# Kernel tuning notes

Hardware: AMD Instinct MI355X
Metric: run time of the kernel (lower is better)

## Reference

```python
import jax, jax.numpy as jnp
import numpy as np

B = 1024        # batch
S = 2048        # nsampled + 1 (index 0 is the positive label)
E = 128         # emb_size
V = 100000      # vocab = len(tags_weight)


def setup_inputs() -> dict:
    key = jax.random.key(0)
    k1, k2, k3, k4 = jax.random.split(key, 4)
    inputs = jax.random.normal(k1, (B, E), dtype=jnp.float32)
    weight = jax.random.normal(k2, (V, E), dtype=jnp.float32)
    bias = jax.random.normal(k3, (V,), dtype=jnp.float32)
    sample_ids = jax.random.randint(k4, (B, S), 0, V)  # column 0 = positive label
    return {"inputs": inputs, "weight": weight, "bias": bias, "sample_ids": sample_ids}


def reference(inputs, weight, bias, sample_ids):
    # Gather sampled rows: [B, S, E] and [B, S]
    sample_weights = weight[sample_ids]
    sample_bias = bias[sample_ids]
    # Batched dot: logits[b, s] = <inputs[b], sample_weights[b, s]> + bias
    logits = jnp.einsum('be,bse->bs', inputs, sample_weights) + sample_bias
    # CrossEntropyLoss with targets all-zero (positive class is at index 0), mean reduction
    loss = jnp.mean(jax.nn.logsumexp(logits, axis=-1) - logits[:, 0])
    return loss
```

## Files before the change

kernel.cpp:

```cpp
#include <hip/hip_runtime.h>
#include <float.h>
#include <math.h>

#define BATCH 1024
#define NS    2048
#define EMB   128
#define VOCAB 100000
#define THREADS 256

#define PARTS 8
#define PSIZE (VOCAB / PARTS)

#define FCHUNKS 8
#define FSCHUNK (NS / FCHUNKS)
#define ITERSF (FSCHUNK / 64)

#define KSHIFT 40.0f
#define INVB   (1.0f / (float)BATCH)


typedef float floatx2 __attribute__((ext_vector_type(2)));

#if __has_builtin(__builtin_amdgcn_cvt_pk_f32_fp8) && __has_builtin(__builtin_amdgcn_cvt_pk_fp8_f32)
#define USE_FP8_BUILTINS 1
#else
#define USE_FP8_BUILTINS 0
#include <hip/hip_fp8.h>
#endif

__device__ inline floatx2 cvt2_lo(unsigned int w) {
#if USE_FP8_BUILTINS
    return __builtin_amdgcn_cvt_pk_f32_fp8((int)w, false);
#else
    __hip_fp8_e4m3 a, b;
    a.__x = (unsigned char)(w & 0xff);
    b.__x = (unsigned char)((w >> 8) & 0xff);
    floatx2 r; r.x = (float)a; r.y = (float)b; return r;
#endif
}
__device__ inline floatx2 cvt2_hi(unsigned int w) {
#if USE_FP8_BUILTINS
    return __builtin_amdgcn_cvt_pk_f32_fp8((int)w, true);
#else
    __hip_fp8_e4m3 a, b;
    a.__x = (unsigned char)((w >> 16) & 0xff);
    b.__x = (unsigned char)((w >> 24) & 0xff);
    floatx2 r; r.x = (float)a; r.y = (float)b; return r;
#endif
}
__device__ inline unsigned int pack4_fp8(float4 v) {
#if USE_FP8_BUILTINS
    int w = 0;
    w = __builtin_amdgcn_cvt_pk_fp8_f32(v.x, v.y, w, false);
    w = __builtin_amdgcn_cvt_pk_fp8_f32(v.z, v.w, w, true);
    return (unsigned int)w;
#else
    __hip_fp8_e4m3 h0(v.x), h1(v.y), h2(v.z), h3(v.w);
    return (unsigned int)h0.__x | ((unsigned int)h1.__x << 8)
         | ((unsigned int)h2.__x << 16) | ((unsigned int)h3.__x << 24);
#endif
}

__global__ __launch_bounds__(THREADS) void convert_weights_fp8(
    const float* __restrict__ w, unsigned int* __restrict__ w8)
{
    const size_t i = (size_t)blockIdx.x * THREADS + threadIdx.x;
    const float4* src = (const float4*)w;
    float4 a = src[4 * i + 0];
    float4 b = src[4 * i + 1];
    float4 c = src[4 * i + 2];
    float4 d = src[4 * i + 3];
    uint4 o;
    o.x = pack4_fp8(a);
    o.y = pack4_fp8(b);
    o.z = pack4_fp8(c);
    o.w = pack4_fp8(d);
    ((uint4*)w8)[i] = o;
}

__global__ __launch_bounds__(THREADS, 2) void sampled_ce_partial_p(
    const float*        __restrict__ inputs,
    const unsigned int* __restrict__ w8,
    const float*        __restrict__ bias,
    const int*          __restrict__ sample_ids,
    float* __restrict__ pm,
    float* __restrict__ plogit0)
{
    const int blk = blockIdx.x;
    const int p   = blk & (PARTS - 1);
    const int b   = blk >> 3;
    const int t   = threadIdx.x;
    const int lane = t & 63;
    const int e_part = t & 7;
    const int s_sub  = t >> 3;
    const int lo  = p * PSIZE;

    __shared__ float s_in[EMB];
    __shared__ int   s_ids[NS];
    __shared__ int   s_sel[NS];
    __shared__ float s_red[4];
    __shared__ int   s_cnt;
    __shared__ int   s_pos0;

    if (t < EMB / 4) {
        ((float4*)s_in)[t] = ((const float4*)(inputs + (size_t)b * EMB))[t];
    }
    const int4* ids4 = (const int4*)(sample_ids + (size_t)b * NS);
    ((int4*)s_ids)[t]       = ids4[t];
    ((int4*)s_ids)[t + 256] = ids4[t + 256];
    if (t == 0) { s_cnt = 0; s_pos0 = -1; }
    __syncthreads();

#pragma unroll
    for (int c = 0; c < NS / THREADS; ++c) {
        const int pos = c * THREADS + t;
        const int id  = s_ids[pos];
        const bool pred = ((unsigned)(id - lo)) < (unsigned)PSIZE;
        const unsigned long long mask = __ballot(pred);
        int base;
        if (lane == 0) base = atomicAdd(&s_cnt, (int)__popcll(mask));
        base = __shfl(base, 0, 64);
        if (pred) {
            const int slot = base +
                (int)__popcll(mask & ((1ull << lane) - 1ull));
            s_sel[slot] = id;
            if (pos == 0) s_pos0 = slot;
        }
    }
    __syncthreads();

    const int count = s_cnt;
    const int pos0  = s_pos0;

    floatx2 cin[8];
#pragma unroll
    for (int q = 0; q < 8; ++q) {
        const int base = e_part * 16 + 2 * q;
        cin[q].x = s_in[base];
        cin[q].y = s_in[base + 1];
    }

    float lsum = 0.0f;
    for (int base = 0; base < count; base += 8 * 32) {
        int ids8[8];
#pragma unroll
        for (int it = 0; it < 8; ++it) {
            const int slot = base + it * 32 + s_sub;
            ids8[it] = (slot < count) ? s_sel[slot] : lo;
        }
        uint4 q[8];
#pragma unroll
        for (int it = 0; it < 8; ++it)
            q[it] = ((const uint4*)w8)[(size_t)ids8[it] * 8 + e_part];
        float bv[8];
#pragma unroll
        for (int it = 0; it < 8; ++it) bv[it] = bias[ids8[it]];

#pragma unroll
        for (int it = 0; it < 8; ++it) {
            floatx2 a2 = {0.0f, 0.0f};
            a2 += cvt2_lo(q[it].x) * cin[0];
            a2 += cvt2_hi(q[it].x) * cin[1];
            a2 += cvt2_lo(q[it].y) * cin[2];
            a2 += cvt2_hi(q[it].y) * cin[3];
            a2 += cvt2_lo(q[it].z) * cin[4];
            a2 += cvt2_hi(q[it].z) * cin[5];
            a2 += cvt2_lo(q[it].w) * cin[6];
            a2 += cvt2_hi(q[it].w) * cin[7];
            float a = a2.x + a2.y;
            a += __shfl_xor(a, 1, 64);
            a += __shfl_xor(a, 2, 64);
            a += __shfl_xor(a, 4, 64);
            const float logit = a + bv[it];
            const int slot = base + it * 32 + s_sub;
            if (slot < count) {
                lsum += __expf(logit - KSHIFT);
                if (slot == pos0 && e_part == 0) plogit0[b] = logit;
            }
        }
    }

#pragma unroll
    for (int off = 1; off < 64; off <<= 1) lsum += __shfl_xor(lsum, off, 64);
    const int wave = t >> 6;
    if ((t & 63) == 0) s_red[wave] = lsum;
    __syncthreads();
    if (t == 0) {
        pm[blk] = (s_red[0] + s_red[1] + s_red[2] + s_red[3]) * 0.125f;
    }
}

__global__ __launch_bounds__(1024) void sampled_ce_finalize_8(
    const float* __restrict__ pm,
    const float* __restrict__ plogit0,
    float* __restrict__ out)
{
    const int t = threadIdx.x;

    const float4* p4 = (const float4*)(pm + (size_t)t * PARTS);
    const float4 p0 = p4[0];
    const float4 p1 = p4[1];
    const float S = (p0.x + p0.y + p0.z + p0.w) + (p1.x + p1.y + p1.z + p1.w);
    float v = (KSHIFT + __logf(S) - plogit0[t]) * INVB;

#pragma unroll
    for (int off = 1; off < 64; off <<= 1) v += __shfl_xor(v, off, 64);

    __shared__ float s[16];
    if ((t & 63) == 0) s[t >> 6] = v;
    __syncthreads();

    if (t == 0) {
        float sum = 0.0f;
#pragma unroll
        for (int w = 0; w < 16; ++w) sum += s[w];
        out[0] = sum;
    }
}

__global__ __launch_bounds__(THREADS) void sampled_ce_partial_f(
    const float* __restrict__ inputs,
    const float* __restrict__ weight,
    const float* __restrict__ bias,
    const int*   __restrict__ sample_ids,
    float* __restrict__ pm,
    float* __restrict__ pl,
    float* __restrict__ plogit0)
{
    const int blk   = blockIdx.x;
    const int b     = blk >> 3;
    const int chunk = blk & (FCHUNKS - 1);
    const int t = threadIdx.x;
    const int e_part  = t & 3;
    const int s_local = t >> 2;

    __shared__ float s_in[EMB];
    __shared__ float s_red[8];

    if (t < EMB / 4) {
        ((float4*)s_in)[t] = ((const float4*)(inputs + (size_t)b * EMB))[t];
    }
    const int* ids_row = sample_ids + (size_t)b * NS + chunk * FSCHUNK;
    int ids[ITERSF];
#pragma unroll
    for (int it = 0; it < ITERSF; ++it) ids[it] = ids_row[it * 64 + s_local];
    __syncthreads();

    float4 cin[8];
#pragma unroll
    for (int k = 0; k < 8; ++k) cin[k] = ((const float4*)s_in)[k * 4 + e_part];

    float m = -FLT_MAX, l = 0.0f;
#pragma unroll
    for (int it = 0; it < ITERSF; ++it) {
        const int id = ids[it];
        const float4* wr = (const float4*)(weight + (size_t)id * EMB);
        float acc = 0.0f;
#pragma unroll
        for (int k = 0; k < 8; ++k) {
            float4 w = wr[k * 4 + e_part];
            acc += w.x * cin[k].x + w.y * cin[k].y + w.z * cin[k].z + w.w * cin[k].w;
        }
        acc += __shfl_xor(acc, 1, 64);
        acc += __shfl_xor(acc, 2, 64);
        const float logit = acc + bias[id];
        const float nm = fmaxf(m, logit);
        l = l * __expf(m - nm) + __expf(logit - nm);
        m = nm;
        if (chunk == 0 && it == 0 && t == 0) plogit0[b] = logit;
    }
    if (e_part != 0) { m = -FLT_MAX; l = 0.0f; }
#pragma unroll
    for (int off = 1; off < 64; off <<= 1) {
        const float om = __shfl_xor(m, off, 64);
        const float ol = __shfl_xor(l, off, 64);
        const float nm = fmaxf(m, om);
        l = l * __expf(m - nm) + ol * __expf(om - nm);
        m = nm;
    }
    const int wave = t >> 6;
    if ((t & 63) == 0) { s_red[wave * 2] = m; s_red[wave * 2 + 1] = l; }
    __syncthreads();
    if (t == 0) {
        float M = s_red[0], L = s_red[1];
#pragma unroll
        for (int w = 1; w < 4; ++w) {
            const float om = s_red[w * 2], ol = s_red[w * 2 + 1];
            const float nm = fmaxf(M, om);
            L = L * __expf(M - nm) + ol * __expf(om - nm);
            M = nm;
        }
        pm[blk] = M;
        pl[blk] = L;
    }
}

__global__ __launch_bounds__(1024) void sampled_ce_finalize_f(
    const float* __restrict__ pm,
    const float* __restrict__ pl,
    const float* __restrict__ plogit0,
    float* __restrict__ out)
{
    const int t = threadIdx.x;
    float M = pm[t * FCHUNKS + 0];
    float L = pl[t * FCHUNKS + 0];
#pragma unroll
    for (int c = 1; c < FCHUNKS; ++c) {
        const float om = pm[t * FCHUNKS + c];
        const float ol = pl[t * FCHUNKS + c];
        const float nm = fmaxf(M, om);
        L = L * __expf(M - nm) + ol * __expf(om - nm);
        M = nm;
    }
    float v = (M + __logf(L) - plogit0[t]) * INVB;
#pragma unroll
    for (int off = 1; off < 64; off <<= 1) v += __shfl_xor(v, off, 64);
    __shared__ float s[16];
    if ((t & 63) == 0) s[t >> 6] = v;
    __syncthreads();
    if (t == 0) {
        float sum = 0.0f;
#pragma unroll
        for (int w = 0; w < 16; ++w) sum += s[w];
        out[0] = sum;
    }
}

extern "C" void kernel_launch(void* const* d_in, const int* in_sizes, int n_in,
                              void* d_out, int out_size, void* d_ws, size_t ws_size,
                              hipStream_t stream) {
    const float* inputs     = (const float*)d_in[0];
    const float* weight     = (const float*)d_in[1];
    const float* bias       = (const float*)d_in[2];
    const int*   sample_ids = (const int*)d_in[3];
    float* out = (float*)d_out;

    float* ws = (float*)d_ws;
    float* pm      = ws;
    float* plogit0 = ws + BATCH * PARTS;
    float* fb_pm   = ws;
    float* fb_pl   = ws + BATCH * FCHUNKS;
    float* fb_pl0  = ws + 2 * BATCH * FCHUNKS;
    const size_t red_bytes = (size_t)(2 * BATCH * FCHUNKS + BATCH) * sizeof(float);
    const size_t w8_bytes  = (size_t)VOCAB * EMB;
    unsigned int* w8 = (unsigned int*)((char*)d_ws + red_bytes);

    if (ws_size >= red_bytes + w8_bytes) {
        convert_weights_fp8<<<dim3((VOCAB * EMB) / (16 * THREADS)), dim3(THREADS), 0, stream>>>(
            weight, w8);
        sampled_ce_partial_p<<<dim3(BATCH * PARTS), dim3(THREADS), 0, stream>>>(
            inputs, w8, bias, sample_ids, pm, plogit0);
        sampled_ce_finalize_8<<<dim3(1), dim3(1024), 0, stream>>>(pm, plogit0, out);
    } else {
        sampled_ce_partial_f<<<dim3(BATCH * FCHUNKS), dim3(THREADS), 0, stream>>>(
            inputs, weight, bias, sample_ids, fb_pm, fb_pl, fb_pl0);
        sampled_ce_finalize_f<<<dim3(1), dim3(1024), 0, stream>>>(fb_pm, fb_pl, fb_pl0, out);
    }
}
```

Baseline: 146.6 us.

## Pre-bucket sample ids by vocab partition in a separate kernel

Adds a bucket_ids kernel that reads each row's sample ids once and scatters them into per-partition lists in global memory, along with counts and the position of the positive label. The partial kernel then loads only its own partition's list instead of scanning all 2048 ids with ballot/atomic compaction in every one of the 8 partition blocks. This removes the 8x redundant id reads and compaction work, at the cost of an extra launch, a 64 MB bucketed buffer written and read through global memory, and shared-memory atomics contending on only 8 counters. If the workspace is too small, execution falls back to the fp32 path.

```diff
diff --git a/kernel.cpp b/kernel.cpp
--- a/kernel.cpp
+++ b/kernel.cpp
@@ -78,11 +78,56 @@
     ((uint4*)w8)[i] = o;
 }
 
-__global__ __launch_bounds__(THREADS, 2) void sampled_ce_partial_p(
+__global__ __launch_bounds__(THREADS) void bucket_ids(
+    const int* __restrict__ sample_ids,
+    int* __restrict__ bucketed,
+    int* __restrict__ counts,
+    int* __restrict__ part0,
+    int* __restrict__ pos0)
+{
+    const int b = blockIdx.x;
+    const int t = threadIdx.x;
+
+    __shared__ int s_cnt[PARTS];
+    __shared__ int s_bucket[PARTS][NS];
+
+    if (t < PARTS) s_cnt[t] = 0;
+    __syncthreads();
+
+    const int4* ids4 = (const int4*)(sample_ids + (size_t)b * NS);
+#pragma unroll
+    for (int c = 0; c < 2; ++c) {
+        const int4 v = ids4[c * THREADS + t];
+        const int idv[4] = {v.x, v.y, v.z, v.w};
+#pragma unroll
+        for (int j = 0; j < 4; ++j) {
+            const int id = idv[j];
+            const int p  = (int)((unsigned)id / (unsigned)PSIZE);
+            const int slot = atomicAdd(&s_cnt[p], 1);
+            s_bucket[p][slot] = id;
+            if (c == 0 && t == 0 && j == 0) { part0[b] = p; pos0[b] = slot; }
+        }
+    }
+    __syncthreads();
+
+#pragma unroll
+    for (int p = 0; p < PARTS; ++p) {
+        const int n4 = (s_cnt[p] + 3) >> 2;
+        int4* dst = (int4*)(bucketed + ((size_t)b * PARTS + p) * NS);
+        const int4* src = (const int4*)s_bucket[p];
+        for (int i = t; i < n4; i += THREADS) dst[i] = src[i];
+    }
+    if (t < PARTS) counts[b * PARTS + t] = s_cnt[t];
+}
+
+__global__ __launch_bounds__(THREADS, 2) void sampled_ce_partial_b(
     const float*        __restrict__ inputs,
     const unsigned int* __restrict__ w8,
     const float*        __restrict__ bias,
-    const int*          __restrict__ sample_ids,
+    const int*          __restrict__ bucketed,
+    const int*          __restrict__ counts,
+    const int*          __restrict__ part0arr,
+    const int*          __restrict__ pos0arr,
     float* __restrict__ pm,
     float* __restrict__ plogit0)
 {
@@ -90,47 +135,24 @@
     const int p   = blk & (PARTS - 1);
     const int b   = blk >> 3;
     const int t   = threadIdx.x;
-    const int lane = t & 63;
     const int e_part = t & 7;
     const int s_sub  = t >> 3;
-    const int lo  = p * PSIZE;
 
     __shared__ float s_in[EMB];
-    __shared__ int   s_ids[NS];
-    __shared__ int   s_sel[NS];
+    __shared__ int   s_list[NS];
     __shared__ float s_red[4];
-    __shared__ int   s_cnt;
-    __shared__ int   s_pos0;
+
+    const int n = counts[blk];
 
     if (t < EMB / 4) {
         ((float4*)s_in)[t] = ((const float4*)(inputs + (size_t)b * EMB))[t];
     }
-    const int4* ids4 = (const int4*)(sample_ids + (size_t)b * NS);
-    ((int4*)s_ids)[t]       = ids4[t];
-    ((int4*)s_ids)[t + 256] = ids4[t + 256];
-    if (t == 0) { s_cnt = 0; s_pos0 = -1; }
-    __syncthreads();
-
-#pragma unroll
-    for (int c = 0; c < NS / THREADS; ++c) {
-        const int pos = c * THREADS + t;
-        const int id  = s_ids[pos];
-        const bool pred = ((unsigned)(id - lo)) < (unsigned)PSIZE;
-        const unsigned long long mask = __ballot(pred);
-        int base;
-        if (lane == 0) base = atomicAdd(&s_cnt, (int)__popcll(mask));
-        base = __shfl(base, 0, 64);
-        if (pred) {
-            const int slot = base +
-                (int)__popcll(mask & ((1ull << lane) - 1ull));
-            s_sel[slot] = id;
-            if (pos == 0) s_pos0 = slot;
-        }
-    }
-    __syncthreads();
-
-    const int count = s_cnt;
-    const int pos0  = s_pos0;
+    const int n4 = (n + 3) >> 2;
+    const int4* src = (const int4*)(bucketed + (size_t)blk * NS);
+    for (int i = t; i < n4; i += THREADS) ((int4*)s_list)[i] = src[i];
+    __syncthreads();
+
+    const int mypos0 = (part0arr[b] == p) ? pos0arr[b] : -1;
 
     floatx2 cin[8];
 #pragma unroll
@@ -141,12 +163,12 @@
     }
 
     float lsum = 0.0f;
-    for (int base = 0; base < count; base += 8 * 32) {
+    for (int base = 0; base < n; base += 8 * 32) {
         int ids8[8];
 #pragma unroll
         for (int it = 0; it < 8; ++it) {
             const int slot = base + it * 32 + s_sub;
-            ids8[it] = (slot < count) ? s_sel[slot] : lo;
+            ids8[it] = (slot < n) ? s_list[slot] : p * PSIZE;
         }
         uint4 q[8];
 #pragma unroll
@@ -173,9 +195,9 @@
             a += __shfl_xor(a, 4, 64);
             const float logit = a + bv[it];
             const int slot = base + it * 32 + s_sub;
-            if (slot < count) {
+            if (slot < n) {
                 lsum += __expf(logit - KSHIFT);
-                if (slot == pos0 && e_part == 0) plogit0[b] = logit;
+                if (slot == mypos0 && e_part == 0) plogit0[b] = logit;
             }
         }
     }
@@ -345,11 +367,20 @@
     const size_t w8_bytes  = (size_t)VOCAB * EMB;
     unsigned int* w8 = (unsigned int*)((char*)d_ws + red_bytes);
 
-    if (ws_size >= red_bytes + w8_bytes) {
+    int* bucketed = (int*)((char*)d_ws + red_bytes + w8_bytes);
+    int* counts   = bucketed + (size_t)BATCH * PARTS * NS;
+    int* part0    = counts + BATCH * PARTS;
+    int* pos0     = part0 + BATCH;
+    const size_t bkt_bytes = ((size_t)BATCH * PARTS * NS + BATCH * PARTS + 2 * BATCH)
+                             * sizeof(int);
+
+    if (ws_size >= red_bytes + w8_bytes + bkt_bytes) {
         convert_weights_fp8<<<dim3((VOCAB * EMB) / (16 * THREADS)), dim3(THREADS), 0, stream>>>(
             weight, w8);
-        sampled_ce_partial_p<<<dim3(BATCH * PARTS), dim3(THREADS), 0, stream>>>(
-            inputs, w8, bias, sample_ids, pm, plogit0);
+        bucket_ids<<<dim3(BATCH), dim3(THREADS), 0, stream>>>(
+            sample_ids, bucketed, counts, part0, pos0);
+        sampled_ce_partial_b<<<dim3(BATCH * PARTS), dim3(THREADS), 0, stream>>>(
+            inputs, w8, bias, bucketed, counts, part0, pos0, pm, plogit0);
         sampled_ce_finalize_8<<<dim3(1), dim3(1024), 0, stream>>>(pm, plogit0, out);
     } else {
         sampled_ce_partial_f<<<dim3(BATCH * FCHUNKS), dim3(THREADS), 0, stream>>>(
```

After: 143.7 us. 2.0% less time.
